# Optimization experiments

Hardware: AMD Instinct MI355X
Metric: run time of the kernel (lower is better)

## Reference

```python
import jax, jax.numpy as jnp
import numpy as np

THINK_STEPS = 15
MAX_ANSWER_SZ = 30


def setup_inputs() -> dict:
    key = jax.random.key(0)
    ks = jax.random.split(key, 6)
    V, H, B, SQ = 95, 2048, 256, 162
    s = 1.0 / np.sqrt(H)
    x = jax.random.randint(ks[0], (B, SQ), 0, V, dtype=jnp.int64)
    W_ih = jax.random.uniform(ks[1], (4 * H, V), jnp.float32, -s, s)
    W_hh = jax.random.uniform(ks[2], (4 * H, H), jnp.float32, -s, s)
    b_ih = jax.random.uniform(ks[3], (4 * H,), jnp.float32, -s, s)
    b_hh = jax.random.uniform(ks[4], (4 * H,), jnp.float32, -s, s)
    W_proj = jax.random.uniform(ks[5], (V, H), jnp.float32, -s, s)
    return {"x": x, "W_ih": W_ih, "W_hh": W_hh, "b_ih": b_ih, "b_hh": b_hh, "W_proj": W_proj}


def reference(x, W_ih, W_hh, b_ih, b_hh, W_proj):
    V = W_ih.shape[1]
    H = W_hh.shape[1]
    B = x.shape[0]
    bias = b_ih + b_hh

    def cell(h, c, inp):
        # PyTorch gate order: i, f, g, o
        g = inp @ W_ih.T + h @ W_hh.T + bias  # (B, 4H)
        i, f, gg, o = jnp.split(g, 4, axis=-1)
        c_new = jax.nn.sigmoid(f) * c + jax.nn.sigmoid(i) * jnp.tanh(gg)
        h_new = jax.nn.sigmoid(o) * jnp.tanh(c_new)
        return h_new, c_new

    # Phase 1: consume one-hot question, seq-major (SQ, B, V)
    xs = jax.nn.one_hot(x.T, V, dtype=jnp.float32)
    h0 = jnp.zeros((B, H), jnp.float32)
    c0 = jnp.zeros((B, H), jnp.float32)

    def q_step(carry, xt):
        h, c = carry
        h, c = cell(h, c, xt)
        return (h, c), None

    (h, c), _ = jax.lax.scan(q_step, (h0, c0), xs)
    out_q = h  # `outputs` after question loop; NOT updated during thinking

    # Phase 2: 15 zero-input "thinking" steps (only state updated)
    zero_in = jnp.zeros((B, V), jnp.float32)

    def t_step(carry, _):
        h, c = carry
        h, c = cell(h, c, zero_in)
        return (h, c), None

    (h, c), _ = jax.lax.scan(t_step, (h, c), None, length=THINK_STEPS)

    def a_step(carry, _):
        out, h, c = carry
        logits = out @ W_proj.T  # (B, V)
        h_new, c_new = cell(h, c, logits)
        return (h_new, h_new, c_new), logits

    _, output_seq = jax.lax.scan(a_step, (out_q, h, c), None, length=MAX_ANSWER_SZ - 1)
    return output_seq.reshape(-1, V)  # ((A-1)*B, V)
```

## Files before the change

kernel.cpp:

```cpp
#include <hip/hip_runtime.h>


#define Hdim 2048
#define G4H  8192
#define Bsz  256
#define Vsz  95
#define SQL  162
#define TSTEPS 15
#define ASTEPS 29

typedef signed char i8;
typedef __attribute__((ext_vector_type(4))) int i32x4;

#define S_RANGE 0.0220970869121f
#define SWI (127.0f / S_RANGE)
#define SG  (S_RANGE / (127.0f * 127.0f))

__device__ __forceinline__ float sigm(float x) { return 1.0f / (1.0f + expf(-x)); }

__device__ __forceinline__ void quant2(float xl, i8& q1, i8& q2) {
  float a = rintf(xl);
  q1 = (i8)(int)a;
  q2 = (i8)(int)rintf((xl - a) * 128.0f);
}

#define LGKM_BAR                                            \
  asm volatile("s_waitcnt lgkmcnt(0)" ::: "memory");        \
  __builtin_amdgcn_s_barrier();

__global__ void k_split2(const float* __restrict__ w, i8* __restrict__ w1,
                         i8* __restrict__ w2) {
  for (long i = blockIdx.x * blockDim.x + threadIdx.x; i < (long)G4H * Hdim;
       i += (long)gridDim.x * blockDim.x) {
    int n = (int)(i >> 11), k = (int)(i & 2047);
    long r = (long)((n & 3) * Hdim + (n >> 2));
    float xl = w[r * Hdim + k] * SWI;
    i8 a, b;
    quant2(xl, a, b);
    w1[i] = a;
    w2[i] = b;
  }
}

__global__ void k_prep(const float* __restrict__ W_ih, const float* __restrict__ b_ih,
                       const float* __restrict__ b_hh, float* __restrict__ wihT2,
                       float* __restrict__ bias2, float* __restrict__ hf,
                       i8* __restrict__ h1, i8* __restrict__ h2) {
  int i = blockIdx.x * 256 + threadIdx.x;
  if (i < Vsz * G4H) {
    int v = i / G4H, n = i % G4H;
    int r = (n & 3) * Hdim + (n >> 2);
    wihT2[i] = W_ih[(long)r * Vsz + v];
  }
  if (i < G4H) {
    int r = (i & 3) * Hdim + (i >> 2);
    bias2[i] = b_ih[r] + b_hh[r];
  }
  if (i < Bsz * Hdim) {
    hf[i] = 0.f;
    h1[i] = 0;
    h2[i] = 0;
  }
}

__global__ __launch_bounds__(512) void k_step(
    const i8* __restrict__ a1p, const i8* __restrict__ a2p,
    const i8* __restrict__ b1p, const i8* __restrict__ b2p,
    const float* __restrict__ bias2, const float* __restrict__ wihT2,
    const float* __restrict__ lgp, const int* __restrict__ x, int tstep,
    int xstride, int mode, float* __restrict__ c, float* __restrict__ hf,
    i8* __restrict__ o1, i8* __restrict__ o2) {
  __shared__ __align__(16) i8 SM[98304];

  const int tid = threadIdx.x;
  const int wave = tid >> 6, lane = tid & 63;

  const int lin = blockIdx.x;
  const int lin2 = (lin & 7) * 32 + (lin >> 3);
  const int row0 = (lin2 & 1) * 128;
  const int col0 = (lin2 >> 1) * 64;

  const int wr = wave >> 1, wc = wave & 1;
  const int lr = lane & 15, lc = lane >> 4;

  const i8* gsrc[6];
  i8* wdst[6];
  {
    const int rr = lane >> 2;
    const int koff = ((lane & 3) ^ (rr & 3) ^ ((rr >> 2) & 3)) * 16;
#pragma unroll
    for (int j = 0; j < 6; ++j) {
      int cc = wave * 6 + j;
      int half = cc / 24, c24 = cc % 24;
      const i8* base;
      long rg;
      if (c24 < 8)       { base = a1p; rg = row0 + c24 * 16; }
      else if (c24 < 16) { base = a2p; rg = row0 + (c24 - 8) * 16; }
      else if (c24 < 20) { base = b1p; rg = col0 + (c24 - 16) * 16; }
      else               { base = b2p; rg = col0 + (c24 - 20) * 16; }
      gsrc[j] = base + (rg + rr) * (long)Hdim + half * 64 + koff;
      wdst[j] = SM + cc * 1024 + lane * 16;
    }
  }

  const int sl = (lc ^ (lr & 3) ^ ((lr >> 2) & 3)) * 16;
  int aoff[2], boff[2];
#pragma unroll
  for (int mf = 0; mf < 2; ++mf) aoff[mf] = (wr * 32 + mf * 16 + lr) * 64 + sl;
#pragma unroll
  for (int nf = 0; nf < 2; ++nf) boff[nf] = 16384 + (wc * 32 + nf * 16 + lr) * 64 + sl;

  i32x4 acc1[2][2] = {};
  i32x4 acc2[2][2] = {};
  const char* smb = (const char*)SM;
  i32x4 qA[6], qB[6], qC[6];

#define LOADQ(q, s)                                                   \
  { _Pragma("unroll") for (int j = 0; j < 6; ++j)                     \
        q[j] = *(const i32x4*)(gsrc[j] + (long)(s) * 128); }
#define WRITEQ(q, s)                                                  \
  { _Pragma("unroll") for (int j = 0; j < 6; ++j)                     \
        *(i32x4*)(wdst[j] + (((s) & 1) * 49152)) = q[j]; }

#define HALF(sb)                                                                \
  {                                                                             \
    i32x4 A10 = *(const i32x4*)(sb + aoff[0]);                                  \
    i32x4 A11 = *(const i32x4*)(sb + aoff[1]);                                  \
    i32x4 A20 = *(const i32x4*)(sb + 8192 + aoff[0]);                           \
    i32x4 A21 = *(const i32x4*)(sb + 8192 + aoff[1]);                           \
    i32x4 B10 = *(const i32x4*)(sb + boff[0]);                                  \
    i32x4 B11 = *(const i32x4*)(sb + boff[1]);                                  \
    i32x4 B20 = *(const i32x4*)(sb + 4096 + boff[0]);                           \
    i32x4 B21 = *(const i32x4*)(sb + 4096 + boff[1]);                           \
    __builtin_amdgcn_s_setprio(1);                                              \
    acc1[0][0] = __builtin_amdgcn_mfma_i32_16x16x64_i8(A10, B10, acc1[0][0], 0, 0, 0); \
    acc1[0][1] = __builtin_amdgcn_mfma_i32_16x16x64_i8(A10, B11, acc1[0][1], 0, 0, 0); \
    acc1[1][0] = __builtin_amdgcn_mfma_i32_16x16x64_i8(A11, B10, acc1[1][0], 0, 0, 0); \
    acc1[1][1] = __builtin_amdgcn_mfma_i32_16x16x64_i8(A11, B11, acc1[1][1], 0, 0, 0); \
    acc2[0][0] = __builtin_amdgcn_mfma_i32_16x16x64_i8(A10, B20, acc2[0][0], 0, 0, 0); \
    acc2[0][1] = __builtin_amdgcn_mfma_i32_16x16x64_i8(A10, B21, acc2[0][1], 0, 0, 0); \
    acc2[1][0] = __builtin_amdgcn_mfma_i32_16x16x64_i8(A11, B20, acc2[1][0], 0, 0, 0); \
    acc2[1][1] = __builtin_amdgcn_mfma_i32_16x16x64_i8(A11, B21, acc2[1][1], 0, 0, 0); \
    acc2[0][0] = __builtin_amdgcn_mfma_i32_16x16x64_i8(A20, B10, acc2[0][0], 0, 0, 0); \
    acc2[0][1] = __builtin_amdgcn_mfma_i32_16x16x64_i8(A20, B11, acc2[0][1], 0, 0, 0); \
    acc2[1][0] = __builtin_amdgcn_mfma_i32_16x16x64_i8(A21, B10, acc2[1][0], 0, 0, 0); \
    acc2[1][1] = __builtin_amdgcn_mfma_i32_16x16x64_i8(A21, B11, acc2[1][1], 0, 0, 0); \
    __builtin_amdgcn_s_setprio(0);                                              \
  }

#define COMPUTE(kb)                                         \
  {                                                         \
    const char* sb0 = smb + ((kb) & 1) * 49152;             \
    HALF(sb0);                                              \
    HALF((sb0 + 24576));                                    \
  }

  LOADQ(qA, 0); LOADQ(qB, 1); LOADQ(qC, 2);
  WRITEQ(qA, 0);
  LGKM_BAR;

  for (int t3 = 0; t3 < 4; ++t3) {
    const int kb0 = t3 * 3;
    LOADQ(qA, kb0 + 3); WRITEQ(qB, kb0 + 1); COMPUTE(kb0); LGKM_BAR;
    LOADQ(qB, kb0 + 4); WRITEQ(qC, kb0 + 2); COMPUTE(kb0 + 1); LGKM_BAR;
    LOADQ(qC, kb0 + 5); WRITEQ(qA, kb0 + 3); COMPUTE(kb0 + 2); LGKM_BAR;
  }
  LOADQ(qA, 15); WRITEQ(qB, 13); COMPUTE(12); LGKM_BAR;
  WRITEQ(qC, 14); COMPUTE(13); LGKM_BAR;
  WRITEQ(qA, 15); COMPUTE(14); LGKM_BAR;
  COMPUTE(15);

  __syncthreads();
  float* gt = (float*)SM;
#pragma unroll
  for (int mf = 0; mf < 2; ++mf)
#pragma unroll
    for (int nf = 0; nf < 2; ++nf) {
      int col = wc * 32 + nf * 16 + lr;
#pragma unroll
      for (int i = 0; i < 4; ++i) {
        int row = wr * 32 + mf * 16 + lc * 4 + i;
        gt[row * 68 + col] =
            ((float)acc1[mf][nf][i] + (float)acc2[mf][nf][i] * 0.0078125f) * SG;
      }
    }
  __syncthreads();

  const int h16 = tid & 15;
  const int bl32 = tid >> 4;
  const int hh_g = (col0 >> 2) + h16;
  const float bi = bias2[col0 + 4 * h16 + 0];
  const float bf_ = bias2[col0 + 4 * h16 + 1];
  const float bg_ = bias2[col0 + 4 * h16 + 2];
  const float bo = bias2[col0 + 4 * h16 + 3];

  float ai[4] = {0, 0, 0, 0}, af[4] = {0, 0, 0, 0};
  float ag[4] = {0, 0, 0, 0}, ao[4] = {0, 0, 0, 0};
  if (mode == 2) {
    const float* wv0 = wihT2 + col0 + 4 * h16;
    for (int v = 0; v < Vsz; ++v) {
      const float* w4 = wv0 + (long)v * G4H;
      float w0 = w4[0], w1 = w4[1], w2 = w4[2], w3 = w4[3];
#pragma unroll
      for (int pr = 0; pr < 4; ++pr) {
        float l = lgp[(row0 + pr * 32 + bl32) * Vsz + v];
        ai[pr] += l * w0; af[pr] += l * w1; ag[pr] += l * w2; ao[pr] += l * w3;
      }
    }
  }

#pragma unroll
  for (int pr = 0; pr < 4; ++pr) {
    int brow = pr * 32 + bl32;
    int bg = row0 + brow;
    const float* gr = &gt[brow * 68 + 4 * h16];
    float xi = gr[0] + bi + ai[pr], xf = gr[1] + bf_ + af[pr];
    float xg = gr[2] + bg_ + ag[pr], xo = gr[3] + bo + ao[pr];
    if (mode == 1) {
      int tok = x[(bg * SQL + tstep) * xstride];
      const float* wv = wihT2 + (long)tok * G4H + col0 + 4 * h16;
      xi += wv[0]; xf += wv[1]; xg += wv[2]; xo += wv[3];
    }
    long ci = (long)bg * Hdim + hh_g;
    float cn = sigm(xf) * c[ci] + sigm(xi) * tanhf(xg);
    float hn = sigm(xo) * tanhf(cn);
    c[ci] = cn;
    hf[ci] = hn;
    i8 q1, q2;
    quant2(hn * 127.0f, q1, q2);
    o1[ci] = q1;
    o2[ci] = q2;
  }
#undef LOADQ
#undef WRITEQ
#undef HALF
#undef COMPUTE
}

__global__ __launch_bounds__(256) void k_logits(const float* __restrict__ src,
                                                const float* __restrict__ Wp,
                                                float* __restrict__ lg,
                                                float* __restrict__ outp) {
  const int b0 = blockIdx.x * 4, tid = threadIdx.x;
  const int wv = tid >> 6, ln = tid & 63;

  float4 hreg[4][8];
#pragma unroll
  for (int r = 0; r < 4; ++r) {
    const float4* srcv = (const float4*)(src + (long)(b0 + r) * Hdim);
#pragma unroll
    for (int i = 0; i < 8; ++i) hreg[r][i] = srcv[ln + 64 * i];
  }

  for (int v = wv; v < Vsz; v += 4) {
    const float4* wrow = (const float4*)(Wp + (long)v * Hdim);
    float s0 = 0.f, s1 = 0.f, s2 = 0.f, s3 = 0.f;
#pragma unroll
    for (int i = 0; i < 8; ++i) {
      float4 w = wrow[ln + 64 * i];
      s0 += w.x * hreg[0][i].x + w.y * hreg[0][i].y + w.z * hreg[0][i].z + w.w * hreg[0][i].w;
      s1 += w.x * hreg[1][i].x + w.y * hreg[1][i].y + w.z * hreg[1][i].z + w.w * hreg[1][i].w;
      s2 += w.x * hreg[2][i].x + w.y * hreg[2][i].y + w.z * hreg[2][i].z + w.w * hreg[2][i].w;
      s3 += w.x * hreg[3][i].x + w.y * hreg[3][i].y + w.z * hreg[3][i].z + w.w * hreg[3][i].w;
    }
#pragma unroll
    for (int off = 32; off; off >>= 1) {
      s0 += __shfl_down(s0, off);
      s1 += __shfl_down(s1, off);
      s2 += __shfl_down(s2, off);
      s3 += __shfl_down(s3, off);
    }
    if (ln == 0) {
      lg[(b0 + 0) * Vsz + v] = s0;
      lg[(b0 + 1) * Vsz + v] = s1;
      lg[(b0 + 2) * Vsz + v] = s2;
      lg[(b0 + 3) * Vsz + v] = s3;
      outp[(b0 + 0) * Vsz + v] = s0;
      outp[(b0 + 1) * Vsz + v] = s1;
      outp[(b0 + 2) * Vsz + v] = s2;
      outp[(b0 + 3) * Vsz + v] = s3;
    }
  }
}

extern "C" void kernel_launch(void* const* d_in, const int* in_sizes, int n_in,
                              void* d_out, int out_size, void* d_ws, size_t ws_size,
                              hipStream_t stream) {
  const int* x = (const int*)d_in[0];
  const float* W_ih = (const float*)d_in[1];
  const float* W_hh = (const float*)d_in[2];
  const float* b_ih = (const float*)d_in[3];
  const float* b_hh = (const float*)d_in[4];
  const float* W_proj = (const float*)d_in[5];
  float* out = (float*)d_out;

  int xstride = (in_sizes[0] > Bsz * SQL) ? 2 : 1;

  i8* w1 = (i8*)d_ws;
  i8* w2 = w1 + (long)G4H * Hdim;
  float* wihT2 = (float*)(w2 + (long)G4H * Hdim);
  float* bias2 = wihT2 + (long)Vsz * G4H;
  float* hf = bias2 + G4H;
  float* c = hf + (long)Bsz * Hdim;
  float* outq = c + (long)Bsz * Hdim;
  float* lg = outq + (long)Bsz * Hdim;
  i8* h1A = (i8*)(lg + Bsz * Vsz);
  i8* h2A = h1A + (long)Bsz * Hdim;
  i8* h1B = h2A + (long)Bsz * Hdim;
  i8* h2B = h1B + (long)Bsz * Hdim;

  k_split2<<<4096, 256, 0, stream>>>(W_hh, w1, w2);
  k_prep<<<3040, 256, 0, stream>>>(W_ih, b_ih, b_hh, wihT2, bias2, hf, h1A, h2A);

  hipMemsetAsync(c, 0, (long)Bsz * Hdim * sizeof(float), stream);

  i8* i1[2] = {h1A, h1B};
  i8* i2[2] = {h2A, h2B};
  int pp = 0;

  for (int t = 0; t < SQL; ++t) {
    k_step<<<256, 512, 0, stream>>>(i1[pp], i2[pp], w1, w2, bias2, wihT2,
                                    nullptr, x, t, xstride, 1, c, hf,
                                    i1[pp ^ 1], i2[pp ^ 1]);
    pp ^= 1;
  }
  hipMemcpyAsync(outq, hf, (long)Bsz * Hdim * sizeof(float),
                 hipMemcpyDeviceToDevice, stream);

  for (int t = 0; t < TSTEPS; ++t) {
    k_step<<<256, 512, 0, stream>>>(i1[pp], i2[pp], w1, w2, bias2, wihT2,
                                    nullptr, nullptr, 0, 1, 0, c, hf,
                                    i1[pp ^ 1], i2[pp ^ 1]);
    pp ^= 1;
  }

  for (int s = 0; s < ASTEPS; ++s) {
    const float* src = (s == 0) ? outq : hf;
    k_logits<<<64, 256, 0, stream>>>(src, W_proj, lg, out + (long)s * Bsz * Vsz);
    k_step<<<256, 512, 0, stream>>>(i1[pp], i2[pp], w1, w2, bias2, wihT2,
                                    lg, nullptr, 0, 1, 2, c, hf,
                                    i1[pp ^ 1], i2[pp ^ 1]);
    pp ^= 1;
  }
}
```

Measured before the change: 5.924 ms.

## Load A operands directly from global into registers, staging only B in LDS

The step kernel no longer stages the A tiles (the quantized hidden-state halves) in shared memory. Each wave now loads its own A fragments straight from global memory into registers, double-buffered across k-blocks, and only the B (weight) tiles go through LDS. LDS use drops from 96KB to 36KB, which may allow more blocks per CU, and the LDS write/read traffic for A goes away. The cost is more global loads per wave, since A rows are now fetched by both column waves instead of shared, plus higher register pressure from two 8-entry A buffers.

Result: slower. 8.815 ms (+48.8%).

```diff
diff --git a/kernel.cpp b/kernel.cpp
--- a/kernel.cpp
+++ b/kernel.cpp
@@ -70,7 +70,7 @@
     const float* __restrict__ lgp, const int* __restrict__ x, int tstep,
     int xstride, int mode, float* __restrict__ c, float* __restrict__ hf,
     i8* __restrict__ o1, i8* __restrict__ o2) {
-  __shared__ __align__(16) i8 SM[98304];
+  __shared__ __align__(16) i8 SM[36864];
 
   const int tid = threadIdx.x;
   const int wave = tid >> 6, lane = tid & 63;
@@ -83,55 +83,62 @@
   const int wr = wave >> 1, wc = wave & 1;
   const int lr = lane & 15, lc = lane >> 4;
 
-  const i8* gsrc[6];
-  i8* wdst[6];
+  const i8* aBase[4];
+  {
+    long arow = (long)(row0 + wr * 32 + lr);
+    aBase[0] = a1p + arow * Hdim + lc * 16;
+    aBase[1] = a1p + (arow + 16) * Hdim + lc * 16;
+    aBase[2] = a2p + arow * Hdim + lc * 16;
+    aBase[3] = a2p + (arow + 16) * Hdim + lc * 16;
+  }
+
+  const i8* gsrc[2];
+  i8* wdst[2];
   {
     const int rr = lane >> 2;
     const int koff = ((lane & 3) ^ (rr & 3) ^ ((rr >> 2) & 3)) * 16;
 #pragma unroll
-    for (int j = 0; j < 6; ++j) {
-      int cc = wave * 6 + j;
-      int half = cc / 24, c24 = cc % 24;
-      const i8* base;
-      long rg;
-      if (c24 < 8)       { base = a1p; rg = row0 + c24 * 16; }
-      else if (c24 < 16) { base = a2p; rg = row0 + (c24 - 8) * 16; }
-      else if (c24 < 20) { base = b1p; rg = col0 + (c24 - 16) * 16; }
-      else               { base = b2p; rg = col0 + (c24 - 20) * 16; }
-      gsrc[j] = base + (rg + rr) * (long)Hdim + half * 64 + koff;
-      wdst[j] = SM + cc * 1024 + lane * 16;
+    for (int j = 0; j < 2; ++j) {
+      int cc = wave * 2 + j;
+      int half = cc >> 3, lev = (cc >> 2) & 1, q = cc & 3;
+      const i8* base = lev ? b2p : b1p;
+      gsrc[j] = base + (long)(col0 + q * 16 + rr) * Hdim + half * 64 + koff;
+      wdst[j] = SM + half * 8192 + lev * 4096 + q * 1024 + lane * 16;
     }
   }
 
   const int sl = (lc ^ (lr & 3) ^ ((lr >> 2) & 3)) * 16;
-  int aoff[2], boff[2];
-#pragma unroll
-  for (int mf = 0; mf < 2; ++mf) aoff[mf] = (wr * 32 + mf * 16 + lr) * 64 + sl;
-#pragma unroll
-  for (int nf = 0; nf < 2; ++nf) boff[nf] = 16384 + (wc * 32 + nf * 16 + lr) * 64 + sl;
+  int boff[2];
+#pragma unroll
+  for (int nf = 0; nf < 2; ++nf) boff[nf] = (wc * 32 + nf * 16 + lr) * 64 + sl;
 
   i32x4 acc1[2][2] = {};
   i32x4 acc2[2][2] = {};
   const char* smb = (const char*)SM;
-  i32x4 qA[6], qB[6], qC[6];
+  i32x4 q0[2], q1[2], aR0[8], aR1[8];
 
 #define LOADQ(q, s)                                                   \
-  { _Pragma("unroll") for (int j = 0; j < 6; ++j)                     \
+  { _Pragma("unroll") for (int j = 0; j < 2; ++j)                     \
         q[j] = *(const i32x4*)(gsrc[j] + (long)(s) * 128); }
 #define WRITEQ(q, s)                                                  \
-  { _Pragma("unroll") for (int j = 0; j < 6; ++j)                     \
-        *(i32x4*)(wdst[j] + (((s) & 1) * 49152)) = q[j]; }
-
-#define HALF(sb)                                                                \
+  { _Pragma("unroll") for (int j = 0; j < 2; ++j)                     \
+        *(i32x4*)(wdst[j] + (((s) & 1) * 16384)) = q[j]; }
+#define LOADA(ar, s)                                                  \
+  { _Pragma("unroll") for (int h = 0; h < 2; ++h)                     \
+      _Pragma("unroll") for (int u = 0; u < 4; ++u)                   \
+        ar[h * 4 + u] = *(const i32x4*)(aBase[u] + (s) * 128 + h * 64); }
+
+#define HALF(h, sb, ar)                                                         \
   {                                                                             \
-    i32x4 A10 = *(const i32x4*)(sb + aoff[0]);                                  \
-    i32x4 A11 = *(const i32x4*)(sb + aoff[1]);                                  \
-    i32x4 A20 = *(const i32x4*)(sb + 8192 + aoff[0]);                           \
-    i32x4 A21 = *(const i32x4*)(sb + 8192 + aoff[1]);                           \
-    i32x4 B10 = *(const i32x4*)(sb + boff[0]);                                  \
-    i32x4 B11 = *(const i32x4*)(sb + boff[1]);                                  \
-    i32x4 B20 = *(const i32x4*)(sb + 4096 + boff[0]);                           \
-    i32x4 B21 = *(const i32x4*)(sb + 4096 + boff[1]);                           \
+    i32x4 A10 = ar[h * 4 + 0];                                                  \
+    i32x4 A11 = ar[h * 4 + 1];                                                  \
+    i32x4 A20 = ar[h * 4 + 2];                                                  \
+    i32x4 A21 = ar[h * 4 + 3];                                                  \
+    const char* sb2 = (sb) + h * 8192;                                          \
+    i32x4 B10 = *(const i32x4*)(sb2 + boff[0]);                                 \
+    i32x4 B11 = *(const i32x4*)(sb2 + boff[1]);                                 \
+    i32x4 B20 = *(const i32x4*)(sb2 + 4096 + boff[0]);                          \
+    i32x4 B21 = *(const i32x4*)(sb2 + 4096 + boff[1]);                          \
     __builtin_amdgcn_s_setprio(1);                                              \
     acc1[0][0] = __builtin_amdgcn_mfma_i32_16x16x64_i8(A10, B10, acc1[0][0], 0, 0, 0); \
     acc1[0][1] = __builtin_amdgcn_mfma_i32_16x16x64_i8(A10, B11, acc1[0][1], 0, 0, 0); \
@@ -148,27 +155,37 @@
     __builtin_amdgcn_s_setprio(0);                                              \
   }
 
-#define COMPUTE(kb)                                         \
+#define COMPUTE(kb, ar)                                     \
   {                                                         \
-    const char* sb0 = smb + ((kb) & 1) * 49152;             \
-    HALF(sb0);                                              \
-    HALF((sb0 + 24576));                                    \
-  }
-
-  LOADQ(qA, 0); LOADQ(qB, 1); LOADQ(qC, 2);
-  WRITEQ(qA, 0);
+    const char* sb0 = smb + ((kb) & 1) * 16384;             \
+    HALF(0, sb0, ar);                                       \
+    HALF(1, sb0, ar);                                       \
+  }
+
+  LOADA(aR0, 0);
+  LOADQ(q0, 0);
+  LOADQ(q1, 1);
+  WRITEQ(q0, 0);
+  LOADA(aR1, 1);
   LGKM_BAR;
 
-  for (int t3 = 0; t3 < 4; ++t3) {
-    const int kb0 = t3 * 3;
-    LOADQ(qA, kb0 + 3); WRITEQ(qB, kb0 + 1); COMPUTE(kb0); LGKM_BAR;
-    LOADQ(qB, kb0 + 4); WRITEQ(qC, kb0 + 2); COMPUTE(kb0 + 1); LGKM_BAR;
-    LOADQ(qC, kb0 + 5); WRITEQ(qA, kb0 + 3); COMPUTE(kb0 + 2); LGKM_BAR;
-  }
-  LOADQ(qA, 15); WRITEQ(qB, 13); COMPUTE(12); LGKM_BAR;
-  WRITEQ(qC, 14); COMPUTE(13); LGKM_BAR;
-  WRITEQ(qA, 15); COMPUTE(14); LGKM_BAR;
-  COMPUTE(15);
+  for (int t = 0; t < 7; ++t) {
+    const int kb = 2 * t;
+    LOADQ(q0, kb + 2);
+    WRITEQ(q1, kb + 1);
+    COMPUTE(kb, aR0);
+    LOADA(aR0, kb + 2);
+    LGKM_BAR;
+    LOADQ(q1, kb + 3);
+    WRITEQ(q0, kb + 2);
+    COMPUTE(kb + 1, aR1);
+    LOADA(aR1, kb + 3);
+    LGKM_BAR;
+  }
+  WRITEQ(q1, 15);
+  COMPUTE(14, aR0);
+  LGKM_BAR;
+  COMPUTE(15, aR1);
 
   __syncthreads();
   float* gt = (float*)SM;
@@ -226,13 +243,14 @@
     float hn = sigm(xo) * tanhf(cn);
     c[ci] = cn;
     hf[ci] = hn;
-    i8 q1, q2;
-    quant2(hn * 127.0f, q1, q2);
-    o1[ci] = q1;
-    o2[ci] = q2;
+    i8 qa, qb;
+    quant2(hn * 127.0f, qa, qb);
+    o1[ci] = qa;
+    o2[ci] = qb;
   }
 #undef LOADQ
 #undef WRITEQ
+#undef LOADA
 #undef HALF
 #undef COMPUTE
 }
```
